# Kernel optimization log

Measured on AMD Instinct MI355X. Metric: run time of the kernel, lower is better.

Reference implementation:

```python
import jax, jax.numpy as jnp
import numpy as np

N_NODES = 50000
KEEP_PROB = 0.5  # dropout = 0.5


def setup_inputs() -> dict:
    key = jax.random.key(0)
    k1, k2, k3, k4, k5 = jax.random.split(key, 5)
    S, E, DIN, DOUT = 2, 800000, 512, 128
    x = jax.random.normal(k1, (N_NODES, DIN), dtype=jnp.float32)
    weights = jax.random.normal(k2, (S, DIN, DOUT), dtype=jnp.float32) * (1.0 / np.sqrt(DIN))
    adj_rows = jax.random.randint(k3, (S, E), 0, N_NODES, dtype=jnp.int32)
    adj_cols = jax.random.randint(k4, (S, E), 0, N_NODES, dtype=jnp.int32)
    adj_vals = jax.random.uniform(k5, (S, E), dtype=jnp.float32)
    return {"x": x, "weights": weights, "adj_rows": adj_rows,
            "adj_cols": adj_cols, "adj_vals": adj_vals}


def reference(x, weights, adj_rows, adj_cols, adj_vals):
    # Dropout (TF semantics: mask and scale by 1/keep_prob), fixed key for determinism.
    mask = (jax.random.uniform(jax.random.key(42), x.shape) < KEEP_PROB)
    xd = x * mask.astype(x.dtype) / KEEP_PROB
    # Dense GEMM per support: pre_sup[s] = dropout(x) @ W_s  -> [S, N, Dout]
    pre_sup = jnp.einsum('nd,sdo->sno', xd, weights)
    # SpMM per support: out[s] = A_s @ pre_sup[s] with A_s in COO form.
    def spmm(rows, cols, vals, h):
        return jax.ops.segment_sum(vals[:, None] * h[cols], rows,
                                   num_segments=N_NODES)
    out = jax.vmap(spmm)(adj_rows, adj_cols, adj_vals, pre_sup)  # [S, N, Dout]
    return jax.nn.relu(out)
```

## Files before the change

### kernel.cpp

```cpp
#include <hip/hip_runtime.h>
#include <stdint.h>

#define N_NODES 50000
#define DIN     512
#define DOUT    128
#define NSUP    2
#define EDGES   800000
#define NEDGE   (NSUP * EDGES)
#define NROWS   (NSUP * N_NODES)
#define NB      782
#define CH      8192
#define NCH     ((NEDGE + CH - 1) / CH)
#define EPT     16
#define SCAP    4096
#define NMASKW  ((N_NODES * DIN) / 32)
#define NMB     1563
#define NWC     256

typedef __attribute__((ext_vector_type(8))) short short8;
typedef __attribute__((ext_vector_type(4))) float f32x4;

__device__ __forceinline__ uint32_t rotl32(uint32_t v, uint32_t d) {
  return (v << d) | (v >> (32u - d));
}

__device__ __forceinline__ void threefry2x32(uint32_t x0, uint32_t x1,
                                             uint32_t& o0, uint32_t& o1) {
  const uint32_t ks0 = 0u;
  const uint32_t ks1 = 42u;
  const uint32_t ks2 = 0u ^ 42u ^ 0x1BD11BDAu;
  x0 += ks0; x1 += ks1;
#define TF_R(r) { x0 += x1; x1 = rotl32(x1, (r)); x1 ^= x0; }
  TF_R(13) TF_R(15) TF_R(26) TF_R(6)
  x0 += ks1; x1 += ks2 + 1u;
  TF_R(17) TF_R(29) TF_R(16) TF_R(24)
  x0 += ks2; x1 += ks0 + 2u;
  TF_R(13) TF_R(15) TF_R(26) TF_R(6)
  x0 += ks0; x1 += ks1 + 3u;
  TF_R(17) TF_R(29) TF_R(16) TF_R(24)
  x0 += ks1; x1 += ks2 + 4u;
  TF_R(13) TF_R(15) TF_R(26) TF_R(6)
  x0 += ks2; x1 += ks0 + 5u;
#undef TF_R
  o0 = x0; o1 = x1;
}

__device__ __forceinline__ bool keep_mask(uint32_t idx) {
  uint32_t o0, o1;
  threefry2x32(0u, idx, o0, o1);
  return ((o0 ^ o1) >> 31) == 0u;
}

__device__ __forceinline__ uint32_t pack_bf16x2(float a, float b) {
  uint32_t ua = __float_as_uint(a), ub = __float_as_uint(b);
  ua += 0x7fffu + ((ua >> 16) & 1u);
  ub += 0x7fffu + ((ub >> 16) & 1u);
  return (ua >> 16) | (ub & 0xffff0000u);
}

__device__ __forceinline__ uint32_t bf16rne(float f) {
  uint32_t u = __float_as_uint(f);
  u += 0x7fffu + ((u >> 16) & 1u);
  return u >> 16;
}

__global__ __launch_bounds__(512) void fused_pre(
    const int* __restrict__ rows, const float* __restrict__ w,
    uint32_t* __restrict__ maskbuf, int* __restrict__ gcnt,
    unsigned short* __restrict__ b16t) {
  const int t  = threadIdx.x;
  const int bb = blockIdx.x;
  if (bb < NCH) {
    __shared__ int hist[NB];
    for (int b = t; b < NB; b += 512) hist[b] = 0;
    __syncthreads();
    int e0 = bb * CH;
#pragma unroll
    for (int i = 0; i < EPT; ++i) {
      int e = e0 + i * 512 + t;
      if (e < NEDGE) {
        int s = (e >= EDGES) ? 1 : 0;
        int grow = s * N_NODES + rows[e];
        atomicAdd(&hist[grow >> 7], 1);
      }
    }
    __syncthreads();
    for (int b = t; b < NB; b += 512)
      if (hist[b]) atomicAdd(&gcnt[b], hist[b]);
  } else if (bb < NCH + NMB) {
    int wid = (bb - NCH) * 512 + t;
    if (wid < NMASKW) {
      uint32_t base = (uint32_t)wid * 32u;
      uint32_t m = 0u;
#pragma unroll 8
      for (int j = 0; j < 32; ++j)
        m |= (keep_mask(base + j) ? 1u : 0u) << j;
      maskbuf[wid] = m;
    }
  } else {
    int i = (bb - NCH - NMB) * 512 + t;
    if (i < NSUP * DIN * DOUT) {
      int s   = i >> 16;
      int rem = i & 65535;
      int k   = rem >> 7;
      int o   = rem & 127;
      b16t[(size_t)(s * DOUT + o) * DIN + k] = (unsigned short)bf16rne(w[i]);
    }
  }
}

__device__ __forceinline__ short8 conv8(float4 a, float4 b, uint32_t bits) {
  float f[8] = {a.x, a.y, a.z, a.w, b.x, b.y, b.z, b.w};
  union { uint32_t u[4]; short8 s; } pk;
#pragma unroll
  for (int q = 0; q < 8; ++q)
    f[q] = ((bits >> q) & 1u) ? f[q] * 2.0f : 0.0f;
#pragma unroll
  for (int q = 0; q < 4; ++q) pk.u[q] = pack_bf16x2(f[2 * q], f[2 * q + 1]);
  return pk.s;
}

__global__ __launch_bounds__(256) void gemm_mfma5(
    const float* __restrict__ x, const uint32_t* __restrict__ maskbuf,
    const unsigned short* __restrict__ b16t,
    unsigned short* __restrict__ pre16) {
  __shared__ unsigned short Bs[256 * 64];
  const int t    = threadIdx.x;
  const int lane = t & 63;
  const int w    = t >> 6;
  const int m0   = blockIdx.x * 64;
  const int rowa = m0 + w * 16 + (lane & 15);
  const int rowc = rowa < N_NODES ? rowa : N_NODES - 1;
  const int k8   = (lane >> 4) * 8;
  const float* xrow = x + (size_t)rowc * DIN;
  const int mrow = rowc * 16;

  f32x4 acc[16];
#pragma unroll
  for (int i = 0; i < 16; ++i) acc[i] = (f32x4){0.f, 0.f, 0.f, 0.f};

  float4 pa[2][2][2];
  uint32_t pmw[2][2];

  const int colb = w * 64 + (lane >> 3);
  const uint32_t ksw = (uint32_t)(((lane & 7) ^ (lane >> 3)) << 3);

#define LOADA(KC, S)                                                          \
  {                                                                           \
    const float4* a0_ = reinterpret_cast<const float4*>(xrow + (KC) + k8);    \
    pa[S][0][0] = a0_[0];                                                     \
    pa[S][0][1] = a0_[1];                                                     \
    const float4* a1_ =                                                       \
        reinterpret_cast<const float4*>(xrow + (KC) + 32 + k8);               \
    pa[S][1][0] = a1_[0];                                                     \
    pa[S][1][1] = a1_[1];                                                     \
    pmw[S][0] = maskbuf[mrow + ((KC) >> 5)];                                  \
    pmw[S][1] = maskbuf[mrow + ((KC) >> 5) + 1];                              \
  }

  LOADA(0, 0);

#pragma unroll
  for (int kc8 = 0; kc8 < 8; ++kc8) {
    const int kc = kc8 * 64;
    asm volatile("s_waitcnt lgkmcnt(0)" ::: "memory");
    __builtin_amdgcn_s_barrier();
#pragma unroll
    for (int i = 0; i < 8; ++i) {
      const unsigned short* g =
          b16t + (size_t)(colb + i * 8) * DIN + kc + ksw;
      __builtin_amdgcn_global_load_lds((const void*)g,
                                       (void*)(&Bs[w * 4096 + i * 512]),
                                       16, 0, 0);
    }
    __builtin_amdgcn_sched_barrier(0);
    if (kc8 < 7) {
      if ((kc8 & 1) == 0) { LOADA(kc + 64, 1); }
      else                { LOADA(kc + 64, 0); }
    }
    __builtin_amdgcn_sched_barrier(0);
    if (kc8 < 7) { asm volatile("s_waitcnt vmcnt(5)" ::: "memory"); }
    else         { asm volatile("s_waitcnt vmcnt(0)" ::: "memory"); }
    __builtin_amdgcn_s_barrier();

    short8 a0, a1;
    if ((kc8 & 1) == 0) {
      a0 = conv8(pa[0][0][0], pa[0][0][1], pmw[0][0] >> k8);
      a1 = conv8(pa[0][1][0], pa[0][1][1], pmw[0][1] >> k8);
    } else {
      a0 = conv8(pa[1][0][0], pa[1][0][1], pmw[1][0] >> k8);
      a1 = conv8(pa[1][1][0], pa[1][1][1], pmw[1][1] >> k8);
    }
#pragma unroll
    for (int nf = 0; nf < 16; ++nf) {
      int col  = nf * 16 + (lane & 15);
      int base = col * 64 + ((lane >> 4) * 8);
      int sw   = (col & 7) << 3;
      short8 b0 = *reinterpret_cast<const short8*>(&Bs[base ^ sw]);
      short8 b1 = *reinterpret_cast<const short8*>(&Bs[(base + 32) ^ sw]);
      acc[nf] = __builtin_amdgcn_mfma_f32_16x16x32_bf16(a0, b0, acc[nf], 0, 0, 0);
      acc[nf] = __builtin_amdgcn_mfma_f32_16x16x32_bf16(a1, b1, acc[nf], 0, 0, 0);
    }
  }
#undef LOADA

  const int rb = m0 + w * 16 + ((lane >> 4) * 4);
#pragma unroll
  for (int nf = 0; nf < 16; ++nf) {
    int col = nf * 16 + (lane & 15);
    int s = col >> 7, o = col & 127;
#pragma unroll
    for (int q = 0; q < 4; ++q) {
      int row = rb + q;
      if (row < N_NODES)
        pre16[(size_t)(s * N_NODES + row) * DOUT + o] =
            (unsigned short)bf16rne(acc[nf][q]);
    }
  }
}

__global__ __launch_bounds__(1024) void scan782(const int* __restrict__ gcnt,
                                                int* __restrict__ bstart,
                                                int* __restrict__ gcursor) {
  __shared__ int sm[1024];
  int t = threadIdx.x;
  int c = (t < NB) ? gcnt[t] : 0;
  sm[t] = c;
  __syncthreads();
  for (int d = 1; d < 1024; d <<= 1) {
    int v = sm[t];
    int a = (t >= d) ? sm[t - d] : 0;
    __syncthreads();
    sm[t] = v + a;
    __syncthreads();
  }
  if (t < NB) {
    int ex = sm[t] - c;
    bstart[t] = ex;
    gcursor[t] = ex;
  }
  if (t == NB - 1) bstart[NB] = sm[t];
}

__global__ __launch_bounds__(512) void bin_scatter(
    const int* __restrict__ rows, const int* __restrict__ cols,
    const float* __restrict__ vals, int* __restrict__ gcursor,
    uint64_t* __restrict__ binned) {
  __shared__ uint32_t hist[NB];
  __shared__ uint32_t hexcl[NB];
  __shared__ uint32_t sbase[NB];
  __shared__ uint32_t scanb[512];
  __shared__ uint64_t ordered[CH];
  __shared__ uint16_t bk16[CH];
  int t = threadIdx.x;
  for (int b = t; b < NB; b += 512) hist[b] = 0;
  __syncthreads();
  int e0 = blockIdx.x * CH;
  uint32_t key[EPT], rank[EPT], bkt[EPT], vbits[EPT];
#pragma unroll
  for (int i = 0; i < EPT; ++i) {
    int e = e0 + i * 512 + t;
    if (e < NEDGE) {
      int s = (e >= EDGES) ? 1 : 0;
      uint32_t grow = (uint32_t)(s * N_NODES + rows[e]);
      uint32_t gcol = (uint32_t)(s * N_NODES + cols[e]);
      vbits[i] = __float_as_uint(vals[e]);
      uint32_t b = grow >> 7;
      bkt[i] = b;
      key[i] = ((grow & 127u) << 17) | gcol;
      rank[i] = atomicAdd(&hist[b], 1u);
    } else {
      bkt[i] = 0xFFFFFFFFu;
    }
  }
  __syncthreads();
  int t2 = t * 2;
  uint32_t a0 = (t2 < NB) ? hist[t2] : 0u;
  uint32_t a1 = (t2 + 1 < NB) ? hist[t2 + 1] : 0u;
  scanb[t] = a0 + a1;
  __syncthreads();
  for (int d = 1; d < 512; d <<= 1) {
    uint32_t v = scanb[t];
    uint32_t a = (t >= d) ? scanb[t - d] : 0u;
    __syncthreads();
    scanb[t] = v + a;
    __syncthreads();
  }
  uint32_t base  = t ? scanb[t - 1] : 0u;
  uint32_t total = scanb[511];
  if (t2 < NB)     hexcl[t2]     = base;
  if (t2 + 1 < NB) hexcl[t2 + 1] = base + a0;
  for (int b = t; b < NB; b += 512)
    if (hist[b]) sbase[b] = (uint32_t)atomicAdd(&gcursor[b], (int)hist[b]);
  __syncthreads();
#pragma unroll
  for (int i = 0; i < EPT; ++i) {
    if (bkt[i] != 0xFFFFFFFFu) {
      uint32_t slot = hexcl[bkt[i]] + rank[i];
      ordered[slot] = ((uint64_t)vbits[i] << 32) | key[i];
      bk16[slot] = (uint16_t)bkt[i];
    }
  }
  __syncthreads();
#pragma unroll
  for (int i = 0; i < EPT; ++i) {
    uint32_t slot = (uint32_t)(i * 512 + t);
    if (slot < total) {
      uint32_t b = bk16[slot];
      uint32_t dst = sbase[b] + (slot - hexcl[b]);
      binned[dst] = ordered[slot];
    }
  }
}

__global__ __launch_bounds__(512) void spmm_sort_pull(
    const int* __restrict__ bstart, const uint64_t* __restrict__ binned,
    const uint32_t* __restrict__ preu, float* __restrict__ out) {
  __shared__ uint64_t ordered[SCAP];
  __shared__ uint32_t hist[128];
  __shared__ uint32_t excl[128];
  const int t = threadIdx.x;
  const int b = blockIdx.x;
  const int beg = bstart[b], end = bstart[b + 1];
  const int cnt = end - beg;
  if (t < 128) hist[t] = 0;
  __syncthreads();
  uint64_t ed[8];
  uint32_t rk[8], rw[8];
#pragma unroll
  for (int i = 0; i < 8; ++i) {
    int slot = i * 512 + t;
    if (slot < cnt) {
      uint64_t e = binned[beg + slot];
      ed[i] = e;
      uint32_t rowin = ((uint32_t)e >> 17) & 127u;
      rw[i] = rowin;
      rk[i] = atomicAdd(&hist[rowin], 1u);
    } else {
      rw[i] = 0xFFFFFFFFu;
    }
  }
  __syncthreads();
  if (t < 128) excl[t] = hist[t];
  __syncthreads();
  for (int d = 1; d < 128; d <<= 1) {
    uint32_t v = (t < 128) ? excl[t] : 0u;
    uint32_t a = (t >= d && t < 128) ? excl[t - d] : 0u;
    __syncthreads();
    if (t < 128) excl[t] = v + a;
    __syncthreads();
  }
  if (t < 128) excl[t] -= hist[t];
  __syncthreads();
#pragma unroll
  for (int i = 0; i < 8; ++i)
    if (rw[i] != 0xFFFFFFFFu)
      ordered[excl[rw[i]] + rk[i]] = ed[i];
  __syncthreads();

  const int lane = t & 63, wave = t >> 6;
  for (int r8 = 0; r8 < 16; ++r8) {
    int r = wave * 16 + r8;
    int grow = b * 128 + r;
    if (grow >= NROWS) break;
    int jbeg = excl[r];
    int jend = jbeg + (int)hist[r];
    float a0 = 0.f, a1 = 0.f;
    int j = jbeg;
    for (; j + 4 <= jend; j += 4) {
      uint64_t e0 = ordered[j],     e1 = ordered[j + 1];
      uint64_t e2 = ordered[j + 2], e3 = ordered[j + 3];
      uint32_t q0 = preu[(size_t)((uint32_t)e0 & 0x1FFFFu) * 64 + lane];
      uint32_t q1 = preu[(size_t)((uint32_t)e1 & 0x1FFFFu) * 64 + lane];
      uint32_t q2 = preu[(size_t)((uint32_t)e2 & 0x1FFFFu) * 64 + lane];
      uint32_t q3 = preu[(size_t)((uint32_t)e3 & 0x1FFFFu) * 64 + lane];
      float v0 = __uint_as_float((uint32_t)(e0 >> 32));
      float v1 = __uint_as_float((uint32_t)(e1 >> 32));
      float v2 = __uint_as_float((uint32_t)(e2 >> 32));
      float v3 = __uint_as_float((uint32_t)(e3 >> 32));
      a0 += v0 * __uint_as_float(q0 << 16);
      a1 += v0 * __uint_as_float(q0 & 0xffff0000u);
      a0 += v1 * __uint_as_float(q1 << 16);
      a1 += v1 * __uint_as_float(q1 & 0xffff0000u);
      a0 += v2 * __uint_as_float(q2 << 16);
      a1 += v2 * __uint_as_float(q2 & 0xffff0000u);
      a0 += v3 * __uint_as_float(q3 << 16);
      a1 += v3 * __uint_as_float(q3 & 0xffff0000u);
    }
    for (; j < jend; ++j) {
      uint64_t e = ordered[j];
      uint32_t q = preu[(size_t)((uint32_t)e & 0x1FFFFu) * 64 + lane];
      float v = __uint_as_float((uint32_t)(e >> 32));
      a0 += v * __uint_as_float(q << 16);
      a1 += v * __uint_as_float(q & 0xffff0000u);
    }
    float2 o = make_float2(fmaxf(a0, 0.f), fmaxf(a1, 0.f));
    *reinterpret_cast<float2*>(out + (size_t)grow * DOUT + 2 * lane) = o;
  }
}

extern "C" void kernel_launch(void* const* d_in, const int* in_sizes, int n_in,
                              void* d_out, int out_size, void* d_ws, size_t ws_size,
                              hipStream_t stream) {
  const float* x    = (const float*)d_in[0];
  const float* w    = (const float*)d_in[1];
  const int*   rows = (const int*)d_in[2];
  const int*   cols = (const int*)d_in[3];
  const float* vals = (const float*)d_in[4];
  float* out = (float*)d_out;

  uint32_t* base = (uint32_t*)d_ws;
  uint32_t* preu       = base;
  unsigned short* b16t = (unsigned short*)(base + 6400000);
  uint32_t* maskbuf    = base + 6400000 + 65536;
  int* gcnt      = (int*)(base + 6400000 + 65536 + 800000);
  int* bstart    = gcnt + 800;
  int* gcursor   = bstart + 800;
  uint64_t* binned = (uint64_t*)(gcursor + 800);
  size_t need = ((size_t)6400000 + 65536 + 800000 + 2400 + 3200000) * 4;
  if (ws_size < need) return;

  hipMemsetAsync(gcnt, 0, NB * sizeof(int), stream);

  fused_pre<<<NCH + NMB + NWC, 512, 0, stream>>>(rows, w, maskbuf, gcnt, b16t);
  scan782<<<1, 1024, 0, stream>>>(gcnt, bstart, gcursor);
  bin_scatter<<<NCH, 512, 0, stream>>>(rows, cols, vals, gcursor, binned);

  gemm_mfma5<<<(N_NODES + 63) / 64, 256, 0, stream>>>(x, maskbuf, b16t,
                                                      (unsigned short*)preu);

  spmm_sort_pull<<<NB, 512, 0, stream>>>(bstart, binned, preu, out);
}
```

Before: 193.0 us.

## Fuse edge binning with GEMM and compute dropout mask per tile in LDS

Merges the bin_scatter and GEMM kernels into one launch, with block ranges dispatching to either edge binning (now 4096-edge chunks) or a 128-row GEMM tile using 512 threads. The dropout mask is no longer precomputed into a global buffer. Each GEMM block generates its mask bits with threefry into LDS, which removes a global mask write and read and one kernel boundary. The catch is that both roles now share a 52KB LDS allocation, which may limit occupancy, and every GEMM block carries the threefry compute.

```diff
diff --git a/kernel.cpp b/kernel.cpp
--- a/kernel.cpp
+++ b/kernel.cpp
@@ -12,9 +12,11 @@
 #define CH      8192
 #define NCH     ((NEDGE + CH - 1) / CH)
 #define EPT     16
+#define CH4     4096
+#define NCH4    ((NEDGE + CH4 - 1) / CH4)
+#define EPT4    8
 #define SCAP    4096
-#define NMASKW  ((N_NODES * DIN) / 32)
-#define NMB     1563
+#define GB      ((N_NODES + 127) / 128)
 #define NWC     256
 
 typedef __attribute__((ext_vector_type(8))) short short8;
@@ -64,10 +66,20 @@
   return u >> 16;
 }
 
-__global__ __launch_bounds__(512) void fused_pre(
+__device__ __forceinline__ short8 conv8(float4 a, float4 b, uint32_t bits) {
+  float f[8] = {a.x, a.y, a.z, a.w, b.x, b.y, b.z, b.w};
+  union { uint32_t u[4]; short8 s; } pk;
+#pragma unroll
+  for (int q = 0; q < 8; ++q)
+    f[q] = ((bits >> q) & 1u) ? f[q] * 2.0f : 0.0f;
+#pragma unroll
+  for (int q = 0; q < 4; ++q) pk.u[q] = pack_bf16x2(f[2 * q], f[2 * q + 1]);
+  return pk.s;
+}
+
+__global__ __launch_bounds__(512) void fused_pre2(
     const int* __restrict__ rows, const float* __restrict__ w,
-    uint32_t* __restrict__ maskbuf, int* __restrict__ gcnt,
-    unsigned short* __restrict__ b16t) {
+    int* __restrict__ gcnt, unsigned short* __restrict__ b16t) {
   const int t  = threadIdx.x;
   const int bb = blockIdx.x;
   if (bb < NCH) {
@@ -87,18 +99,8 @@
     __syncthreads();
     for (int b = t; b < NB; b += 512)
       if (hist[b]) atomicAdd(&gcnt[b], hist[b]);
-  } else if (bb < NCH + NMB) {
-    int wid = (bb - NCH) * 512 + t;
-    if (wid < NMASKW) {
-      uint32_t base = (uint32_t)wid * 32u;
-      uint32_t m = 0u;
-#pragma unroll 8
-      for (int j = 0; j < 32; ++j)
-        m |= (keep_mask(base + j) ? 1u : 0u) << j;
-      maskbuf[wid] = m;
-    }
   } else {
-    int i = (bb - NCH - NMB) * 512 + t;
+    int i = (bb - NCH) * 512 + t;
     if (i < NSUP * DIN * DOUT) {
       int s   = i >> 16;
       int rem = i & 65535;
@@ -109,41 +111,140 @@
   }
 }
 
-__device__ __forceinline__ short8 conv8(float4 a, float4 b, uint32_t bits) {
-  float f[8] = {a.x, a.y, a.z, a.w, b.x, b.y, b.z, b.w};
-  union { uint32_t u[4]; short8 s; } pk;
-#pragma unroll
-  for (int q = 0; q < 8; ++q)
-    f[q] = ((bits >> q) & 1u) ? f[q] * 2.0f : 0.0f;
-#pragma unroll
-  for (int q = 0; q < 4; ++q) pk.u[q] = pack_bf16x2(f[2 * q], f[2 * q + 1]);
-  return pk.s;
-}
-
-__global__ __launch_bounds__(256) void gemm_mfma5(
-    const float* __restrict__ x, const uint32_t* __restrict__ maskbuf,
-    const unsigned short* __restrict__ b16t,
+__global__ __launch_bounds__(1024) void scan782(const int* __restrict__ gcnt,
+                                                int* __restrict__ bstart,
+                                                int* __restrict__ gcursor) {
+  __shared__ int sm[1024];
+  int t = threadIdx.x;
+  int c = (t < NB) ? gcnt[t] : 0;
+  sm[t] = c;
+  __syncthreads();
+  for (int d = 1; d < 1024; d <<= 1) {
+    int v = sm[t];
+    int a = (t >= d) ? sm[t - d] : 0;
+    __syncthreads();
+    sm[t] = v + a;
+    __syncthreads();
+  }
+  if (t < NB) {
+    int ex = sm[t] - c;
+    bstart[t] = ex;
+    gcursor[t] = ex;
+  }
+  if (t == NB - 1) bstart[NB] = sm[t];
+}
+
+__global__ __launch_bounds__(512) void fused_main(
+    const int* __restrict__ rows, const int* __restrict__ cols,
+    const float* __restrict__ vals, int* __restrict__ gcursor,
+    uint64_t* __restrict__ binned,
+    const float* __restrict__ x, const unsigned short* __restrict__ b16t,
     unsigned short* __restrict__ pre16) {
-  __shared__ unsigned short Bs[256 * 64];
-  const int t    = threadIdx.x;
+  __shared__ uint8_t smem[53248];
+  const int t  = threadIdx.x;
+  const int bb = blockIdx.x;
+
+  if (bb < NCH4) {
+    uint64_t* ordered = (uint64_t*)smem;
+    uint16_t* bk16    = (uint16_t*)(smem + 32768);
+    uint32_t* hist    = (uint32_t*)(smem + 40960);
+    uint32_t* hexcl   = (uint32_t*)(smem + 44088);
+    uint32_t* sbase   = (uint32_t*)(smem + 47216);
+    uint32_t* scanb   = (uint32_t*)(smem + 50344);
+    for (int b = t; b < NB; b += 512) hist[b] = 0;
+    __syncthreads();
+    int e0 = bb * CH4;
+    uint32_t key[EPT4], rank[EPT4], bkt[EPT4], vbits[EPT4];
+#pragma unroll
+    for (int i = 0; i < EPT4; ++i) {
+      int e = e0 + i * 512 + t;
+      if (e < NEDGE) {
+        int s = (e >= EDGES) ? 1 : 0;
+        uint32_t grow = (uint32_t)(s * N_NODES + rows[e]);
+        uint32_t gcol = (uint32_t)(s * N_NODES + cols[e]);
+        vbits[i] = __float_as_uint(vals[e]);
+        uint32_t b = grow >> 7;
+        bkt[i] = b;
+        key[i] = ((grow & 127u) << 17) | gcol;
+        rank[i] = atomicAdd(&hist[b], 1u);
+      } else {
+        bkt[i] = 0xFFFFFFFFu;
+      }
+    }
+    __syncthreads();
+    int t2 = t * 2;
+    uint32_t a0 = (t2 < NB) ? hist[t2] : 0u;
+    uint32_t a1 = (t2 + 1 < NB) ? hist[t2 + 1] : 0u;
+    scanb[t] = a0 + a1;
+    __syncthreads();
+    for (int d = 1; d < 512; d <<= 1) {
+      uint32_t v = scanb[t];
+      uint32_t a = (t >= d) ? scanb[t - d] : 0u;
+      __syncthreads();
+      scanb[t] = v + a;
+      __syncthreads();
+    }
+    uint32_t base  = t ? scanb[t - 1] : 0u;
+    uint32_t total = scanb[511];
+    if (t2 < NB)     hexcl[t2]     = base;
+    if (t2 + 1 < NB) hexcl[t2 + 1] = base + a0;
+    for (int b = t; b < NB; b += 512)
+      if (hist[b]) sbase[b] = (uint32_t)atomicAdd(&gcursor[b], (int)hist[b]);
+    __syncthreads();
+#pragma unroll
+    for (int i = 0; i < EPT4; ++i) {
+      if (bkt[i] != 0xFFFFFFFFu) {
+        uint32_t slot = hexcl[bkt[i]] + rank[i];
+        ordered[slot] = ((uint64_t)vbits[i] << 32) | key[i];
+        bk16[slot] = (uint16_t)bkt[i];
+      }
+    }
+    __syncthreads();
+#pragma unroll
+    for (int i = 0; i < EPT4; ++i) {
+      uint32_t slot = (uint32_t)(i * 512 + t);
+      if (slot < total) {
+        uint32_t b = bk16[slot];
+        uint32_t dst = sbase[b] + (slot - hexcl[b]);
+        binned[dst] = ordered[slot];
+      }
+    }
+    return;
+  }
+
+  unsigned short* Bs = (unsigned short*)smem;
+  uint32_t* mlds     = (uint32_t*)(smem + 32768);
   const int lane = t & 63;
   const int w    = t >> 6;
-  const int m0   = blockIdx.x * 64;
+  const int m0   = (bb - NCH4) * 128;
+
+#pragma unroll
+  for (int i = 0; i < 4; ++i) {
+    int id = i * 512 + t;
+    int r  = id & 127;
+    int j  = id >> 7;
+    uint32_t ebase = (uint32_t)(m0 + r) * 512u + (uint32_t)j * 32u;
+    uint32_t m = 0u;
+#pragma unroll 8
+    for (int q = 0; q < 32; ++q)
+      m |= (keep_mask(ebase + q) ? 1u : 0u) << q;
+    mlds[j * 128 + r] = m;
+  }
+  __syncthreads();
+
   const int rowa = m0 + w * 16 + (lane & 15);
   const int rowc = rowa < N_NODES ? rowa : N_NODES - 1;
   const int k8   = (lane >> 4) * 8;
+  const int rl   = w * 16 + (lane & 15);
   const float* xrow = x + (size_t)rowc * DIN;
-  const int mrow = rowc * 16;
 
   f32x4 acc[16];
 #pragma unroll
   for (int i = 0; i < 16; ++i) acc[i] = (f32x4){0.f, 0.f, 0.f, 0.f};
 
   float4 pa[2][2][2];
-  uint32_t pmw[2][2];
-
-  const int colb = w * 64 + (lane >> 3);
-  const uint32_t ksw = (uint32_t)(((lane & 7) ^ (lane >> 3)) << 3);
+
+  const uint32_t ksw_lane = (uint32_t)(t & 7);
 
 #define LOADA(KC, S)                                                          \
   {                                                                           \
@@ -154,8 +255,6 @@
         reinterpret_cast<const float4*>(xrow + (KC) + 32 + k8);               \
     pa[S][1][0] = a1_[0];                                                     \
     pa[S][1][1] = a1_[1];                                                     \
-    pmw[S][0] = maskbuf[mrow + ((KC) >> 5)];                                  \
-    pmw[S][1] = maskbuf[mrow + ((KC) >> 5) + 1];                              \
   }
 
   LOADA(0, 0);
@@ -166,12 +265,14 @@
     asm volatile("s_waitcnt lgkmcnt(0)" ::: "memory");
     __builtin_amdgcn_s_barrier();
 #pragma unroll
-    for (int i = 0; i < 8; ++i) {
+    for (int i = 0; i < 4; ++i) {
+      int slot = i * 512 + t;
+      int col  = slot >> 3;
+      int kgrp = slot & 7;
       const unsigned short* g =
-          b16t + (size_t)(colb + i * 8) * DIN + kc + ksw;
-      __builtin_amdgcn_global_load_lds((const void*)g,
-                                       (void*)(&Bs[w * 4096 + i * 512]),
-                                       16, 0, 0);
+          b16t + (size_t)col * DIN + kc + ((kgrp ^ (col & 7)) << 3);
+      __builtin_amdgcn_global_load_lds(
+          (const void*)g, (void*)(&Bs[(i * 512 + w * 64) * 8]), 16, 0, 0);
     }
     __builtin_amdgcn_sched_barrier(0);
     if (kc8 < 7) {
@@ -179,17 +280,19 @@
       else                { LOADA(kc + 64, 0); }
     }
     __builtin_amdgcn_sched_barrier(0);
-    if (kc8 < 7) { asm volatile("s_waitcnt vmcnt(5)" ::: "memory"); }
+    if (kc8 < 7) { asm volatile("s_waitcnt vmcnt(4)" ::: "memory"); }
     else         { asm volatile("s_waitcnt vmcnt(0)" ::: "memory"); }
     __builtin_amdgcn_s_barrier();
 
+    uint32_t bits0 = mlds[(kc8 * 2 + 0) * 128 + rl] >> k8;
+    uint32_t bits1 = mlds[(kc8 * 2 + 1) * 128 + rl] >> k8;
     short8 a0, a1;
     if ((kc8 & 1) == 0) {
-      a0 = conv8(pa[0][0][0], pa[0][0][1], pmw[0][0] >> k8);
-      a1 = conv8(pa[0][1][0], pa[0][1][1], pmw[0][1] >> k8);
+      a0 = conv8(pa[0][0][0], pa[0][0][1], bits0);
+      a1 = conv8(pa[0][1][0], pa[0][1][1], bits1);
     } else {
-      a0 = conv8(pa[1][0][0], pa[1][0][1], pmw[1][0] >> k8);
-      a1 = conv8(pa[1][1][0], pa[1][1][1], pmw[1][1] >> k8);
+      a0 = conv8(pa[1][0][0], pa[1][0][1], bits0);
+      a1 = conv8(pa[1][1][0], pa[1][1][1], bits1);
     }
 #pragma unroll
     for (int nf = 0; nf < 16; ++nf) {
@@ -215,100 +318,6 @@
       if (row < N_NODES)
         pre16[(size_t)(s * N_NODES + row) * DOUT + o] =
             (unsigned short)bf16rne(acc[nf][q]);
-    }
-  }
-}
-
-__global__ __launch_bounds__(1024) void scan782(const int* __restrict__ gcnt,
-                                                int* __restrict__ bstart,
-                                                int* __restrict__ gcursor) {
-  __shared__ int sm[1024];
-  int t = threadIdx.x;
-  int c = (t < NB) ? gcnt[t] : 0;
-  sm[t] = c;
-  __syncthreads();
-  for (int d = 1; d < 1024; d <<= 1) {
-    int v = sm[t];
-    int a = (t >= d) ? sm[t - d] : 0;
-    __syncthreads();
-    sm[t] = v + a;
-    __syncthreads();
-  }
-  if (t < NB) {
-    int ex = sm[t] - c;
-    bstart[t] = ex;
-    gcursor[t] = ex;
-  }
-  if (t == NB - 1) bstart[NB] = sm[t];
-}
-
-__global__ __launch_bounds__(512) void bin_scatter(
-    const int* __restrict__ rows, const int* __restrict__ cols,
-    const float* __restrict__ vals, int* __restrict__ gcursor,
-    uint64_t* __restrict__ binned) {
-  __shared__ uint32_t hist[NB];
-  __shared__ uint32_t hexcl[NB];
-  __shared__ uint32_t sbase[NB];
-  __shared__ uint32_t scanb[512];
-  __shared__ uint64_t ordered[CH];
-  __shared__ uint16_t bk16[CH];
-  int t = threadIdx.x;
-  for (int b = t; b < NB; b += 512) hist[b] = 0;
-  __syncthreads();
-  int e0 = blockIdx.x * CH;
-  uint32_t key[EPT], rank[EPT], bkt[EPT], vbits[EPT];
-#pragma unroll
-  for (int i = 0; i < EPT; ++i) {
-    int e = e0 + i * 512 + t;
-    if (e < NEDGE) {
-      int s = (e >= EDGES) ? 1 : 0;
-      uint32_t grow = (uint32_t)(s * N_NODES + rows[e]);
-      uint32_t gcol = (uint32_t)(s * N_NODES + cols[e]);
-      vbits[i] = __float_as_uint(vals[e]);
-      uint32_t b = grow >> 7;
-      bkt[i] = b;
-      key[i] = ((grow & 127u) << 17) | gcol;
-      rank[i] = atomicAdd(&hist[b], 1u);
-    } else {
-      bkt[i] = 0xFFFFFFFFu;
-    }
-  }
-  __syncthreads();
-  int t2 = t * 2;
-  uint32_t a0 = (t2 < NB) ? hist[t2] : 0u;
-  uint32_t a1 = (t2 + 1 < NB) ? hist[t2 + 1] : 0u;
-  scanb[t] = a0 + a1;
-  __syncthreads();
-  for (int d = 1; d < 512; d <<= 1) {
-    uint32_t v = scanb[t];
-    uint32_t a = (t >= d) ? scanb[t - d] : 0u;
-    __syncthreads();
-    scanb[t] = v + a;
-    __syncthreads();
-  }
-  uint32_t base  = t ? scanb[t - 1] : 0u;
-  uint32_t total = scanb[511];
-  if (t2 < NB)     hexcl[t2]     = base;
-  if (t2 + 1 < NB) hexcl[t2 + 1] = base + a0;
-  for (int b = t; b < NB; b += 512)
-    if (hist[b]) sbase[b] = (uint32_t)atomicAdd(&gcursor[b], (int)hist[b]);
-  __syncthreads();
-#pragma unroll
-  for (int i = 0; i < EPT; ++i) {
-    if (bkt[i] != 0xFFFFFFFFu) {
-      uint32_t slot = hexcl[bkt[i]] + rank[i];
-      ordered[slot] = ((uint64_t)vbits[i] << 32) | key[i];
-      bk16[slot] = (uint16_t)bkt[i];
-    }
-  }
-  __syncthreads();
-#pragma unroll
-  for (int i = 0; i < EPT; ++i) {
-    uint32_t slot = (uint32_t)(i * 512 + t);
-    if (slot < total) {
-      uint32_t b = bk16[slot];
-      uint32_t dst = sbase[b] + (slot - hexcl[b]);
-      binned[dst] = ordered[slot];
     }
   }
 }
@@ -412,22 +421,18 @@
   uint32_t* base = (uint32_t*)d_ws;
   uint32_t* preu       = base;
   unsigned short* b16t = (unsigned short*)(base + 6400000);
-  uint32_t* maskbuf    = base + 6400000 + 65536;
-  int* gcnt      = (int*)(base + 6400000 + 65536 + 800000);
+  int* gcnt      = (int*)(base + 6400000 + 65536);
   int* bstart    = gcnt + 800;
   int* gcursor   = bstart + 800;
   uint64_t* binned = (uint64_t*)(gcursor + 800);
-  size_t need = ((size_t)6400000 + 65536 + 800000 + 2400 + 3200000) * 4;
+  size_t need = ((size_t)6400000 + 65536 + 2400 + 3200000) * 4;
   if (ws_size < need) return;
 
   hipMemsetAsync(gcnt, 0, NB * sizeof(int), stream);
 
-  fused_pre<<<NCH + NMB + NWC, 512, 0, stream>>>(rows, w, maskbuf, gcnt, b16t);
+  fused_pre2<<<NCH + NWC, 512, 0, stream>>>(rows, w, gcnt, b16t);
   scan782<<<1, 1024, 0, stream>>>(gcnt, bstart, gcursor);
-  bin_scatter<<<NCH, 512, 0, stream>>>(rows, cols, vals, gcursor, binned);
-
-  gemm_mfma5<<<(N_NODES + 63) / 64, 256, 0, stream>>>(x, maskbuf, b16t,
-                                                      (unsigned short*)preu);
-
+  fused_main<<<NCH4 + GB, 512, 0, stream>>>(rows, cols, vals, gcursor, binned,
+                                            x, b16t, (unsigned short*)preu);
   spmm_sort_pull<<<NB, 512, 0, stream>>>(bstart, binned, preu, out);
 }
```

Result: slower. 213.0 us (+10.4%).

## Pre-swizzle weights into MFMA fragment order and read B directly from global

Applied to the files above, without the earlier changes.

The weight conversion now writes bf16 weights in the exact per-lane MFMA fragment order, so the GEMM kernel loads B operands straight from global memory (L2/L1-cached) with coalesced 16-byte reads. The LDS staging buffer, the global_load_lds copies and both per-iteration barriers are removed. This trades shared-memory reuse and explicit latency hiding for reliance on cache hits across waves, and the B loads now sit on the critical path with no explicit prefetch.

```diff
diff --git a/kernel.cpp b/kernel.cpp
--- a/kernel.cpp
+++ b/kernel.cpp
@@ -64,10 +64,21 @@
   return u >> 16;
 }
 
+__device__ __forceinline__ short8 conv8(float4 a, float4 b, uint32_t bits) {
+  float f[8] = {a.x, a.y, a.z, a.w, b.x, b.y, b.z, b.w};
+  union { uint32_t u[4]; short8 s; } pk;
+#pragma unroll
+  for (int q = 0; q < 8; ++q)
+    f[q] = ((bits >> q) & 1u) ? f[q] * 2.0f : 0.0f;
+#pragma unroll
+  for (int q = 0; q < 4; ++q) pk.u[q] = pack_bf16x2(f[2 * q], f[2 * q + 1]);
+  return pk.s;
+}
+
 __global__ __launch_bounds__(512) void fused_pre(
     const int* __restrict__ rows, const float* __restrict__ w,
     uint32_t* __restrict__ maskbuf, int* __restrict__ gcnt,
-    unsigned short* __restrict__ b16t) {
+    unsigned short* __restrict__ b16r) {
   const int t  = threadIdx.x;
   const int bb = blockIdx.x;
   if (bb < NCH) {
@@ -100,31 +111,23 @@
   } else {
     int i = (bb - NCH - NMB) * 512 + t;
     if (i < NSUP * DIN * DOUT) {
-      int s   = i >> 16;
-      int rem = i & 65535;
-      int k   = rem >> 7;
-      int o   = rem & 127;
-      b16t[(size_t)(s * DOUT + o) * DIN + k] = (unsigned short)bf16rne(w[i]);
-    }
-  }
-}
-
-__device__ __forceinline__ short8 conv8(float4 a, float4 b, uint32_t bits) {
-  float f[8] = {a.x, a.y, a.z, a.w, b.x, b.y, b.z, b.w};
-  union { uint32_t u[4]; short8 s; } pk;
-#pragma unroll
-  for (int q = 0; q < 8; ++q)
-    f[q] = ((bits >> q) & 1u) ? f[q] * 2.0f : 0.0f;
-#pragma unroll
-  for (int q = 0; q < 4; ++q) pk.u[q] = pack_bf16x2(f[2 * q], f[2 * q + 1]);
-  return pk.s;
-}
-
-__global__ __launch_bounds__(256) void gemm_mfma5(
+      int j    = i & 7;
+      int lane = (i >> 3) & 63;
+      int kk   = (i >> 9) & 1;
+      int nf   = (i >> 10) & 15;
+      int kc8  = (i >> 14) & 7;
+      int col  = nf * 16 + (lane & 15);
+      int s    = col >> 7, o = col & 127;
+      int k    = kc8 * 64 + kk * 32 + ((lane >> 4) << 3) + j;
+      b16r[i] = (unsigned short)bf16rne(w[((size_t)s * DIN + k) * DOUT + o]);
+    }
+  }
+}
+
+__global__ __launch_bounds__(256) void gemm_flat(
     const float* __restrict__ x, const uint32_t* __restrict__ maskbuf,
-    const unsigned short* __restrict__ b16t,
+    const unsigned short* __restrict__ b16r,
     unsigned short* __restrict__ pre16) {
-  __shared__ unsigned short Bs[256 * 64];
   const int t    = threadIdx.x;
   const int lane = t & 63;
   const int w    = t >> 6;
@@ -141,9 +144,6 @@
 
   float4 pa[2][2][2];
   uint32_t pmw[2][2];
-
-  const int colb = w * 64 + (lane >> 3);
-  const uint32_t ksw = (uint32_t)(((lane & 7) ^ (lane >> 3)) << 3);
 
 #define LOADA(KC, S)                                                          \
   {                                                                           \
@@ -162,27 +162,10 @@
 
 #pragma unroll
   for (int kc8 = 0; kc8 < 8; ++kc8) {
-    const int kc = kc8 * 64;
-    asm volatile("s_waitcnt lgkmcnt(0)" ::: "memory");
-    __builtin_amdgcn_s_barrier();
-#pragma unroll
-    for (int i = 0; i < 8; ++i) {
-      const unsigned short* g =
-          b16t + (size_t)(colb + i * 8) * DIN + kc + ksw;
-      __builtin_amdgcn_global_load_lds((const void*)g,
-                                       (void*)(&Bs[w * 4096 + i * 512]),
-                                       16, 0, 0);
-    }
-    __builtin_amdgcn_sched_barrier(0);
     if (kc8 < 7) {
-      if ((kc8 & 1) == 0) { LOADA(kc + 64, 1); }
-      else                { LOADA(kc + 64, 0); }
-    }
-    __builtin_amdgcn_sched_barrier(0);
-    if (kc8 < 7) { asm volatile("s_waitcnt vmcnt(5)" ::: "memory"); }
-    else         { asm volatile("s_waitcnt vmcnt(0)" ::: "memory"); }
-    __builtin_amdgcn_s_barrier();
-
+      if ((kc8 & 1) == 0) { LOADA(kc8 * 64 + 64, 1); }
+      else                { LOADA(kc8 * 64 + 64, 0); }
+    }
     short8 a0, a1;
     if ((kc8 & 1) == 0) {
       a0 = conv8(pa[0][0][0], pa[0][0][1], pmw[0][0] >> k8);
@@ -191,13 +174,11 @@
       a0 = conv8(pa[1][0][0], pa[1][0][1], pmw[1][0] >> k8);
       a1 = conv8(pa[1][1][0], pa[1][1][1], pmw[1][1] >> k8);
     }
+    const unsigned short* bbase = b16r + (size_t)kc8 * 16384 + lane * 8;
 #pragma unroll
     for (int nf = 0; nf < 16; ++nf) {
-      int col  = nf * 16 + (lane & 15);
-      int base = col * 64 + ((lane >> 4) * 8);
-      int sw   = (col & 7) << 3;
-      short8 b0 = *reinterpret_cast<const short8*>(&Bs[base ^ sw]);
-      short8 b1 = *reinterpret_cast<const short8*>(&Bs[(base + 32) ^ sw]);
+      short8 b0 = *reinterpret_cast<const short8*>(bbase + nf * 1024);
+      short8 b1 = *reinterpret_cast<const short8*>(bbase + nf * 1024 + 512);
       acc[nf] = __builtin_amdgcn_mfma_f32_16x16x32_bf16(a0, b0, acc[nf], 0, 0, 0);
       acc[nf] = __builtin_amdgcn_mfma_f32_16x16x32_bf16(a1, b1, acc[nf], 0, 0, 0);
     }
@@ -411,7 +392,7 @@
 
   uint32_t* base = (uint32_t*)d_ws;
   uint32_t* preu       = base;
-  unsigned short* b16t = (unsigned short*)(base + 6400000);
+  unsigned short* b16r = (unsigned short*)(base + 6400000);
   uint32_t* maskbuf    = base + 6400000 + 65536;
   int* gcnt      = (int*)(base + 6400000 + 65536 + 800000);
   int* bstart    = gcnt + 800;
@@ -422,12 +403,12 @@
 
   hipMemsetAsync(gcnt, 0, NB * sizeof(int), stream);
 
-  fused_pre<<<NCH + NMB + NWC, 512, 0, stream>>>(rows, w, maskbuf, gcnt, b16t);
+  fused_pre<<<NCH + NMB + NWC, 512, 0, stream>>>(rows, w, maskbuf, gcnt, b16r);
   scan782<<<1, 1024, 0, stream>>>(gcnt, bstart, gcursor);
   bin_scatter<<<NCH, 512, 0, stream>>>(rows, cols, vals, gcursor, binned);
 
-  gemm_mfma5<<<(N_NODES + 63) / 64, 256, 0, stream>>>(x, maskbuf, b16t,
-                                                      (unsigned short*)preu);
+  gemm_flat<<<(N_NODES + 63) / 64, 256, 0, stream>>>(x, maskbuf, b16r,
+                                                     (unsigned short*)preu);
 
   spmm_sort_pull<<<NB, 512, 0, stream>>>(bstart, binned, preu, out);
 }
```

Result: slower. 208.3 us (+7.9%).
